# Kernel tuning notes

Measured on AMD Instinct MI355X. Metric: run time of the kernel, lower is better.

The kernel has to match this reference:

```python
import jax, jax.numpy as jnp
import numpy as np

D_MODEL = 1024
NUM_HEADS = 16
D_K = D_MODEL // NUM_HEADS


def setup_inputs() -> dict:
    key = jax.random.key(0)
    ks = jax.random.split(key, 11)
    B, S = 2, 2048
    s = 1.0 / np.sqrt(D_MODEL)
    return {
        "q": jax.random.normal(ks[0], (B, S, D_MODEL), jnp.float32),
        "k": jax.random.normal(ks[1], (B, S, D_MODEL), jnp.float32),
        "v": jax.random.normal(ks[2], (B, S, D_MODEL), jnp.float32),
        "w_q": jax.random.normal(ks[3], (D_MODEL, D_MODEL), jnp.float32) * s,
        "b_q": jnp.zeros((D_MODEL,), jnp.float32),
        "w_k": jax.random.normal(ks[4], (D_MODEL, D_MODEL), jnp.float32) * s,
        "b_k": jnp.zeros((D_MODEL,), jnp.float32),
        "w_v": jax.random.normal(ks[5], (D_MODEL, D_MODEL), jnp.float32) * s,
        "b_v": jnp.zeros((D_MODEL,), jnp.float32),
        "w_o": jax.random.normal(ks[6], (D_MODEL, D_MODEL), jnp.float32) * s,
        "b_o": jnp.zeros((D_MODEL,), jnp.float32),
    }


def reference(q, k, v, w_q, b_q, w_k, b_k, w_v, b_v, w_o, b_o):
    B, S, _ = q.shape
    H, Dk = NUM_HEADS, D_K

    def split_heads(x):  # [B,S,D] -> [B,H,S,Dk]
        return x.reshape(B, S, H, Dk).transpose(0, 2, 1, 3)

    # torch nn.Linear: x @ W.T + b
    qh = split_heads(q @ w_q.T + b_q)
    kh = split_heads(k @ w_k.T + b_k)
    vh = split_heads(v @ w_v.T + b_v)

    scale = 1.0 / jnp.sqrt(jnp.asarray(Dk, qh.dtype))
    scores = jnp.einsum("bhsd,bhtd->bhst", qh, kh) * scale  # [B,H,S,S]
    attn = jax.nn.softmax(scores, axis=-1)
    # dropout is identity in eval/deterministic baseline
    out = jnp.einsum("bhst,bhtd->bhsd", attn, vh)  # [B,H,S,Dk]
    out = out.transpose(0, 2, 1, 3).reshape(B, S, H * Dk)
    return out @ w_o.T + b_o
```

## Files before the change

kernel.cpp:

```cpp
#include <hip/hip_runtime.h>
#include <hip/hip_bf16.h>
#include <stdint.h>

typedef unsigned short u16;
typedef __attribute__((ext_vector_type(8))) short short8;
typedef __attribute__((ext_vector_type(8))) __bf16 bf16x8;
typedef __attribute__((ext_vector_type(4))) float f32x4;
typedef __attribute__((ext_vector_type(4))) uint32_t u32x4;

#if defined(__has_builtin)
#if __has_builtin(__builtin_amdgcn_global_load_lds)
#define USE_GLLDS 1
#endif
#endif

#if defined(__has_builtin)
#if __has_builtin(__builtin_amdgcn_exp2f)
#define HAVE_EXP2_BUILTIN 1
#endif
#endif
__device__ __forceinline__ float fexp2(float x) {
#ifdef HAVE_EXP2_BUILTIN
  return __builtin_amdgcn_exp2f(x);
#else
  return exp2f(x);
#endif
}

__device__ __forceinline__ u16 f2bf(float f) {
  __hip_bfloat16 h = __float2bfloat16(f);
  return __builtin_bit_cast(u16, h);
}

__device__ __forceinline__ f32x4 mfma16(bf16x8 a, bf16x8 b, f32x4 c) {
  return __builtin_amdgcn_mfma_f32_16x16x32_bf16(a, b, c, 0, 0, 0);
}

#ifdef USE_GLLDS
__device__ __forceinline__ void async_cp16(const void* g, void* l) {
  __builtin_amdgcn_global_load_lds(
      (const __attribute__((address_space(1))) void*)g,
      (__attribute__((address_space(3))) void*)l, 16, 0, 0);
}
#endif

__global__ __launch_bounds__(256) void cvt_all(
    const float* __restrict__ q, const float* __restrict__ k,
    const float* __restrict__ v, const float* __restrict__ w0,
    const float* __restrict__ w1, const float* __restrict__ w2,
    const float* __restrict__ w3, u16* __restrict__ dst) {
  size_t i = ((size_t)blockIdx.x * 256 + threadIdx.x) * 8;
  const size_t M1 = 1u << 20;
  const float* s;
  size_t base;
  if (i < 4 * M1) { s = q; base = 0; }
  else if (i < 8 * M1) { s = k; base = 4 * M1; }
  else if (i < 12 * M1) { s = v; base = 8 * M1; }
  else if (i < 13 * M1) { s = w0; base = 12 * M1; }
  else if (i < 14 * M1) { s = w1; base = 13 * M1; }
  else if (i < 15 * M1) { s = w2; base = 14 * M1; }
  else { s = w3; base = 15 * M1; }
  const float4 a = *(const float4*)(s + (i - base));
  const float4 b = *(const float4*)(s + (i - base) + 4);
  short8 r;
  r[0] = (short)f2bf(a.x); r[1] = (short)f2bf(a.y);
  r[2] = (short)f2bf(a.z); r[3] = (short)f2bf(a.w);
  r[4] = (short)f2bf(b.x); r[5] = (short)f2bf(b.y);
  r[6] = (short)f2bf(b.z); r[7] = (short)f2bf(b.w);
  *(short8*)(dst + i) = r;
}

__device__ __forceinline__ void gemm_body(const u16* __restrict__ X,
                                          const u16* __restrict__ W,
                                          const float* __restrict__ bias,
                                          void* __restrict__ outp, int mode) {
  __shared__ u16 Al[128 * 64];
  __shared__ u16 Bl[128 * 64];
  const int tid = threadIdx.x;
  const int wv = tid >> 6, l = tid & 63;
  const int wr = wv >> 1, wc = wv & 1;
  const int m0 = blockIdx.y * 128, n0 = blockIdx.x * 128;
  const int lrow = l & 15, lk = (l >> 4) * 8;

  f32x4 acc[4][4];
#pragma unroll
  for (int i = 0; i < 4; ++i)
#pragma unroll
    for (int j = 0; j < 4; ++j) acc[i][j] = (f32x4){0.f, 0.f, 0.f, 0.f};

  const u16* Asrc = X + (size_t)(m0 + (tid >> 3)) * 1024 + (tid & 7) * 8;
  const u16* Bsrc = W + (size_t)(n0 + (tid >> 3)) * 1024 + (tid & 7) * 8;

  for (int kt = 0; kt < 1024; kt += 64) {
#ifdef USE_GLLDS
#pragma unroll
    for (int p = 0; p < 4; ++p) {
      async_cp16(Asrc + (size_t)p * 32 * 1024 + kt, &Al[p * 2048 + wv * 512]);
      async_cp16(Bsrc + (size_t)p * 32 * 1024 + kt, &Bl[p * 2048 + wv * 512]);
    }
#else
    short8 ar[4], br[4];
#pragma unroll
    for (int p = 0; p < 4; ++p) {
      ar[p] = *(const short8*)(Asrc + (size_t)p * 32 * 1024 + kt);
      br[p] = *(const short8*)(Bsrc + (size_t)p * 32 * 1024 + kt);
    }
#pragma unroll
    for (int p = 0; p < 4; ++p) {
      *(short8*)&Al[p * 2048 + tid * 8] = ar[p];
      *(short8*)&Bl[p * 2048 + tid * 8] = br[p];
    }
#endif
    __syncthreads();
#pragma unroll
    for (int ks = 0; ks < 2; ++ks) {
      bf16x8 af[4], bf[4];
#pragma unroll
      for (int mf = 0; mf < 4; ++mf)
        af[mf] = *(const bf16x8*)&Al[(wr * 64 + mf * 16 + lrow) * 64 + ks * 32 + lk];
#pragma unroll
      for (int nf = 0; nf < 4; ++nf)
        bf[nf] = *(const bf16x8*)&Bl[(wc * 64 + nf * 16 + lrow) * 64 + ks * 32 + lk];
#pragma unroll
      for (int mf = 0; mf < 4; ++mf)
#pragma unroll
        for (int nf = 0; nf < 4; ++nf)
          acc[mf][nf] = mfma16(af[mf], bf[nf], acc[mf][nf]);
    }
    __syncthreads();
  }

  const int rb = (l >> 4) * 4;
#pragma unroll
  for (int mf = 0; mf < 4; ++mf) {
#pragma unroll
    for (int nf = 0; nf < 4; ++nf) {
      const int gn = n0 + wc * 64 + nf * 16 + lrow;
      const float bi = bias[gn];
#pragma unroll
      for (int r = 0; r < 4; ++r) {
        const int gm = m0 + wr * 64 + mf * 16 + rb + r;
        float val = acc[mf][nf][r] + bi;
        const int b = gm >> 11, s = gm & 2047, h = gn >> 6, d = gn & 63;
        if (mode == 3) {
          ((float*)outp)[(size_t)gm * 1024 + gn] = val;
        } else if (mode == 2) {
          ((u16*)outp)[(((size_t)((b * 16 + h) * 64 + d)) << 11) + s] = f2bf(val);
        } else {
          if (mode == 0) val *= 0.18033688f;
          ((u16*)outp)[(((size_t)((b * 16 + h) * 2048 + s)) << 6) + d] = f2bf(val);
        }
      }
    }
  }
}

__global__ __launch_bounds__(256) void gemm_proj(
    const u16* __restrict__ qb, const u16* __restrict__ wqb,
    const float* __restrict__ b_q, const float* __restrict__ b_k,
    const float* __restrict__ b_v, u16* __restrict__ Qh) {
  const int z = blockIdx.z;
  const float* bias = (z == 0) ? b_q : ((z == 1) ? b_k : b_v);
  gemm_body(qb + ((size_t)z << 22), wqb + ((size_t)z << 20), bias,
            Qh + ((size_t)z << 22), z);
}

__global__ __launch_bounds__(256) void gemm_out(
    const u16* __restrict__ X, const u16* __restrict__ W,
    const float* __restrict__ bias, float* __restrict__ out) {
  gemm_body(X, W, bias, out, 3);
}

__global__ __launch_bounds__(512, 4) void flash_attn4(
    const u16* __restrict__ Qh, const u16* __restrict__ Kh,
    const u16* __restrict__ VT, u16* __restrict__ Op,
    float2* __restrict__ ml) {
  __shared__ __align__(16) u16 Kbuf[4096];
  __shared__ __align__(16) u16 Vbuf[4096];
  __shared__ __align__(16) uint32_t Pl[8 * 576];

  const int tid = threadIdx.x;
  const int wv = tid >> 6, l = tid & 63;
  const int q = l & 15, g = l >> 4;

  const int s_lin = blockIdx.x + (blockIdx.y << 4) + (blockIdx.z << 9);
  const int o = ((s_lin & 7) << 7) + (s_lin >> 3);
  const int qt = o & 15, bh = (o >> 4) & 31, z = o >> 9;

  const u16* Qp = Qh + ((size_t)bh * 2048 + qt * 128 + wv * 16) * 64;
  const u16* Kp = Kh + (size_t)bh * 2048 * 64;
  const u16* Vp = VT + (size_t)bh * 64 * 2048;

  bf16x8 qf[2];
  qf[0] = *(const bf16x8*)(Qp + q * 64 + g * 8);
  qf[1] = *(const bf16x8*)(Qp + q * 64 + 32 + g * 8);

  f32x4 o_acc[4];
#pragma unroll
  for (int df = 0; df < 4; ++df) o_acc[df] = (f32x4){0.f, 0.f, 0.f, 0.f};
  float m = -1e30f, ls = 0.f;

  const int srow = l >> 3;
  const int scolq = (l & 7) ^ srow;
  const int pbase = wv * 576 + q * 36;
  const char* kb = (const char*)&Kbuf[0];
  const char* vb = (const char*)&Vbuf[0];
  const int rsw = (q & 7) << 4;

  const u16* kg = Kp + (size_t)(z * 1024 + wv * 8 + srow) * 64 + scolq * 8;
  const u16* vg = Vp + (size_t)(wv * 8 + srow) * 2048 + z * 1024 + scolq * 8;

  {
    short8 k0 = *(const short8*)kg;
    short8 v0 = *(const short8*)vg;
    *(short8*)&Kbuf[wv * 512 + l * 8] = k0;
    *(short8*)&Vbuf[wv * 512 + l * 8] = v0;
  }
  kg += 64 * 64;
  vg += 64;
  __syncthreads();

  for (int tt = 0; tt < 16; ++tt) {
    short8 kr, vr;
    if (tt < 15) {
      kr = *(const short8*)kg;
      vr = *(const short8*)vg;
      kg += 64 * 64;
      vg += 64;
    }

    f32x4 s[4];
#pragma unroll
    for (int nj = 0; nj < 4; ++nj) s[nj] = (f32x4){0.f, 0.f, 0.f, 0.f};
#pragma unroll
    for (int ks = 0; ks < 2; ++ks) {
#pragma unroll
      for (int nj = 0; nj < 4; ++nj) {
        bf16x8 kf = *(const bf16x8*)(kb + (nj * 16 + q) * 128 +
                                     (((ks * 4 + g) << 4) ^ rsw));
        s[nj] = mfma16(kf, qf[ks], s[nj]);
      }
    }

    const float a0 = fmaxf(fmaxf(s[0][0], s[0][1]), fmaxf(s[0][2], s[0][3]));
    const float a1 = fmaxf(fmaxf(s[1][0], s[1][1]), fmaxf(s[1][2], s[1][3]));
    const float a2 = fmaxf(fmaxf(s[2][0], s[2][1]), fmaxf(s[2][2], s[2][3]));
    const float a3 = fmaxf(fmaxf(s[3][0], s[3][1]), fmaxf(s[3][2], s[3][3]));
    float mt = fmaxf(fmaxf(a0, a1), fmaxf(a2, a3));
    mt = fmaxf(mt, __shfl_xor(mt, 16));
    mt = fmaxf(mt, __shfl_xor(mt, 32));
    if (!__all(mt <= m + 8.f)) {
      const float nm = fmaxf(m, mt);
      const float rf = fexp2(m - nm);
      m = nm;
      ls *= rf;
#pragma unroll
      for (int df = 0; df < 4; ++df) o_acc[df] *= rf;
    }
    float ps = 0.f;
#pragma unroll
    for (int nj = 0; nj < 4; ++nj)
#pragma unroll
      for (int r = 0; r < 4; ++r) {
        s[nj][r] = fexp2(s[nj][r] - m);
        ps += s[nj][r];
      }
    ps += __shfl_xor(ps, 16);
    ps += __shfl_xor(ps, 32);
    ls += ps;

#pragma unroll
    for (int nj = 0; nj < 4; ++nj)
#pragma unroll
      for (int pp = 0; pp < 2; ++pp) {
        uint32_t w = (uint32_t)f2bf(s[nj][2 * pp]) |
                     ((uint32_t)f2bf(s[nj][2 * pp + 1]) << 16);
        Pl[pbase + nj * 8 + g * 2 + pp] = w;
      }

#pragma unroll
    for (int ks = 0; ks < 2; ++ks) {
      u32x4 pw = *(const u32x4*)&Pl[pbase + ks * 16 + 4 * g];
      bf16x8 pf = __builtin_bit_cast(bf16x8, pw);
#pragma unroll
      for (int df = 0; df < 4; ++df) {
        bf16x8 vf = *(const bf16x8*)(vb + (df * 16 + q) * 128 +
                                     (((ks * 4 + g) << 4) ^ rsw));
        o_acc[df] = mfma16(vf, pf, o_acc[df]);
      }
    }

    __syncthreads();
    if (tt < 15) {
      *(short8*)&Kbuf[wv * 512 + l * 8] = kr;
      *(short8*)&Vbuf[wv * 512 + l * 8] = vr;
    }
    __syncthreads();
  }

  const float inv = 1.f / ls;
  const int rowb = qt * 128 + wv * 16 + q;
  const size_t prow = (size_t)(z * 32 + bh) * 2048 + rowb;
  u16* Po = Op + (prow << 6);
#pragma unroll
  for (int df = 0; df < 4; ++df)
#pragma unroll
    for (int pp = 0; pp < 2; ++pp) {
      uint32_t w = (uint32_t)f2bf(o_acc[df][2 * pp] * inv) |
                   ((uint32_t)f2bf(o_acc[df][2 * pp + 1] * inv) << 16);
      *(uint32_t*)(Po + df * 16 + 4 * g + 2 * pp) = w;
    }
  if (g == 0) ml[prow] = make_float2(m, ls);
}

__global__ __launch_bounds__(256) void combine(
    const uint32_t* __restrict__ Op32, const float2* __restrict__ ml,
    u16* __restrict__ AO) {
  const int j = blockIdx.x * 256 + threadIdx.x;
  const int rowid = j >> 5, w5 = j & 31;
  const float2 a = ml[rowid];
  const float2 c = ml[(1 << 16) + rowid];
  const float M = fmaxf(a.x, c.x);
  float w1 = a.y * fexp2(a.x - M);
  float w2 = c.y * fexp2(c.x - M);
  const float inv = 1.f / (w1 + w2);
  w1 *= inv;
  w2 *= inv;
  const uint32_t p1 = Op32[j];
  const uint32_t p2 = Op32[(1u << 21) + j];
  const float lo = w1 * __builtin_bit_cast(float, p1 << 16) +
                   w2 * __builtin_bit_cast(float, p2 << 16);
  const float hi = w1 * __builtin_bit_cast(float, p1 & 0xffff0000u) +
                   w2 * __builtin_bit_cast(float, p2 & 0xffff0000u);
  const uint32_t outw = (uint32_t)f2bf(lo) | ((uint32_t)f2bf(hi) << 16);
  const int bh = rowid >> 11, s = rowid & 2047, b = bh >> 4, h = bh & 15;
  ((uint32_t*)AO)[((size_t)(b * 2048 + s) << 9) + h * 32 + w5] = outw;
}

extern "C" void kernel_launch(void* const* d_in, const int* in_sizes, int n_in,
                              void* d_out, int out_size, void* d_ws,
                              size_t ws_size, hipStream_t stream) {
  const float* q = (const float*)d_in[0];
  const float* k = (const float*)d_in[1];
  const float* v = (const float*)d_in[2];
  const float* w_q = (const float*)d_in[3];
  const float* b_q = (const float*)d_in[4];
  const float* w_k = (const float*)d_in[5];
  const float* b_k = (const float*)d_in[6];
  const float* w_v = (const float*)d_in[7];
  const float* b_v = (const float*)d_in[8];
  const float* w_o = (const float*)d_in[9];
  const float* b_o = (const float*)d_in[10];

  u16* ws = (u16*)d_ws;
  u16* qb = ws;
  u16* wqb = ws + (12u << 20);
  u16* wob = ws + (15u << 20);
  u16* Qh = ws + (16u << 20);
  u16* Kh = ws + (20u << 20);
  u16* VT = ws + (24u << 20);
  u16* AO = ws + (28u << 20);
  u16* Op = ws;
  float2* ml = (float2*)(ws + (8u << 20));

  cvt_all<<<dim3(8192), dim3(256), 0, stream>>>(q, k, v, w_q, w_k, w_v, w_o, ws);
  gemm_proj<<<dim3(8, 32, 3), dim3(256), 0, stream>>>(qb, wqb, b_q, b_k, b_v, Qh);
  flash_attn4<<<dim3(16, 32, 2), dim3(512), 0, stream>>>(Qh, Kh, VT, Op, ml);
  combine<<<dim3(8192), dim3(256), 0, stream>>>((const uint32_t*)Op, ml, AO);
  gemm_out<<<dim3(8, 32), dim3(256), 0, stream>>>(AO, wob, b_o, (float*)d_out);
}
```

Measured before the change: 172.2 us.

## Double-buffer GEMM LDS tiles and remap blocks for XCD L2 locality

The projection and output GEMMs now use two LDS buffers, so the next k-tile's global-to-LDS copy is issued before the MFMA work on the current tile. This replaces one of the two barriers per iteration and is meant to hide load latency. The grids are flattened to 1D, and block IDs are remapped so each XCD works on a contiguous patch of M×N tiles, aiming to improve L2 reuse of weights and activations. Launch bounds now request 2 blocks per CU, while doubling LDS to 64 KB per block limits occupancy.

```diff
diff --git a/kernel.cpp b/kernel.cpp
--- a/kernel.cpp
+++ b/kernel.cpp
@@ -70,16 +70,16 @@
   *(short8*)(dst + i) = r;
 }
 
-__device__ __forceinline__ void gemm_body(const u16* __restrict__ X,
+__device__ __forceinline__ void gemm_core(const u16* __restrict__ X,
                                           const u16* __restrict__ W,
                                           const float* __restrict__ bias,
-                                          void* __restrict__ outp, int mode) {
-  __shared__ u16 Al[128 * 64];
-  __shared__ u16 Bl[128 * 64];
+                                          void* __restrict__ outp, int mode,
+                                          int m0, int n0) {
+  __shared__ u16 Al[2][128 * 64];
+  __shared__ u16 Bl[2][128 * 64];
   const int tid = threadIdx.x;
   const int wv = tid >> 6, l = tid & 63;
   const int wr = wv >> 1, wc = wv & 1;
-  const int m0 = blockIdx.y * 128, n0 = blockIdx.x * 128;
   const int lrow = l & 15, lk = (l >> 4) * 8;
 
   f32x4 acc[4][4];
@@ -89,38 +89,53 @@
     for (int j = 0; j < 4; ++j) acc[i][j] = (f32x4){0.f, 0.f, 0.f, 0.f};
 
   const u16* Asrc = X + (size_t)(m0 + (tid >> 3)) * 1024 + (tid & 7) * 8;
-  const u16* Bsrc = W + (size_t)(n0 + (tid >> 3)) * 1024 + (tid & 7) * 8;
+  const u16* Bsrc = W + (size_t)(tid >> 3) * 1024 + (tid & 7) * 8;
+
+#ifdef USE_GLLDS
+#define GSTAGE(buf, kt)                                                       \
+  do {                                                                        \
+    _Pragma("unroll")                                                         \
+    for (int p = 0; p < 4; ++p) {                                             \
+      async_cp16(Asrc + (size_t)p * 32 * 1024 + (kt),                         \
+                 &Al[buf][p * 2048 + wv * 512]);                              \
+      async_cp16(Bsrc + (size_t)p * 32 * 1024 + (kt),                         \
+                 &Bl[buf][p * 2048 + wv * 512]);                              \
+    }                                                                         \
+  } while (0)
+#else
+#define GSTAGE(buf, kt)                                                       \
+  do {                                                                        \
+    short8 ar_[4], br_[4];                                                    \
+    _Pragma("unroll")                                                         \
+    for (int p = 0; p < 4; ++p) {                                             \
+      ar_[p] = *(const short8*)(Asrc + (size_t)p * 32 * 1024 + (kt));         \
+      br_[p] = *(const short8*)(Bsrc + (size_t)p * 32 * 1024 + (kt));         \
+    }                                                                         \
+    _Pragma("unroll")                                                         \
+    for (int p = 0; p < 4; ++p) {                                             \
+      *(short8*)&Al[buf][p * 2048 + tid * 8] = ar_[p];                        \
+      *(short8*)&Bl[buf][p * 2048 + tid * 8] = br_[p];                        \
+    }                                                                         \
+  } while (0)
+#endif
+
+  GSTAGE(0, 0);
+  __syncthreads();
 
   for (int kt = 0; kt < 1024; kt += 64) {
-#ifdef USE_GLLDS
-#pragma unroll
-    for (int p = 0; p < 4; ++p) {
-      async_cp16(Asrc + (size_t)p * 32 * 1024 + kt, &Al[p * 2048 + wv * 512]);
-      async_cp16(Bsrc + (size_t)p * 32 * 1024 + kt, &Bl[p * 2048 + wv * 512]);
-    }
-#else
-    short8 ar[4], br[4];
-#pragma unroll
-    for (int p = 0; p < 4; ++p) {
-      ar[p] = *(const short8*)(Asrc + (size_t)p * 32 * 1024 + kt);
-      br[p] = *(const short8*)(Bsrc + (size_t)p * 32 * 1024 + kt);
-    }
-#pragma unroll
-    for (int p = 0; p < 4; ++p) {
-      *(short8*)&Al[p * 2048 + tid * 8] = ar[p];
-      *(short8*)&Bl[p * 2048 + tid * 8] = br[p];
-    }
-#endif
-    __syncthreads();
+    const int cur = (kt >> 6) & 1;
+    if (kt < 1024 - 64) GSTAGE(cur ^ 1, kt + 64);
 #pragma unroll
     for (int ks = 0; ks < 2; ++ks) {
       bf16x8 af[4], bf[4];
 #pragma unroll
       for (int mf = 0; mf < 4; ++mf)
-        af[mf] = *(const bf16x8*)&Al[(wr * 64 + mf * 16 + lrow) * 64 + ks * 32 + lk];
+        af[mf] = *(const bf16x8*)&Al[cur][(wr * 64 + mf * 16 + lrow) * 64 +
+                                         ks * 32 + lk];
 #pragma unroll
       for (int nf = 0; nf < 4; ++nf)
-        bf[nf] = *(const bf16x8*)&Bl[(wc * 64 + nf * 16 + lrow) * 64 + ks * 32 + lk];
+        bf[nf] = *(const bf16x8*)&Bl[cur][(wc * 64 + nf * 16 + lrow) * 64 +
+                                          ks * 32 + lk];
 #pragma unroll
       for (int mf = 0; mf < 4; ++mf)
 #pragma unroll
@@ -129,6 +144,7 @@
     }
     __syncthreads();
   }
+#undef GSTAGE
 
   const int rb = (l >> 4) * 4;
 #pragma unroll
@@ -155,20 +171,28 @@
   }
 }
 
-__global__ __launch_bounds__(256) void gemm_proj(
+__global__ __launch_bounds__(256, 2) void gemm_proj(
     const u16* __restrict__ qb, const u16* __restrict__ wqb,
     const float* __restrict__ b_q, const float* __restrict__ b_k,
     const float* __restrict__ b_v, u16* __restrict__ Qh) {
-  const int z = blockIdx.z;
+  const int s = blockIdx.x;
+  const int xcd = s & 7, c = s >> 3;
+  const int nx = (xcd >> 2) * 12 + (c % 12);
+  const int my = (xcd & 3) * 8 + (c / 12);
+  const int z = nx >> 3, nxl = nx & 7;
   const float* bias = (z == 0) ? b_q : ((z == 1) ? b_k : b_v);
-  gemm_body(qb + ((size_t)z << 22), wqb + ((size_t)z << 20), bias,
-            Qh + ((size_t)z << 22), z);
-}
-
-__global__ __launch_bounds__(256) void gemm_out(
+  gemm_core(qb + ((size_t)z << 22), wqb + ((size_t)nx << 17), bias,
+            Qh + ((size_t)z << 22), z, my * 128, nxl * 128);
+}
+
+__global__ __launch_bounds__(256, 2) void gemm_out(
     const u16* __restrict__ X, const u16* __restrict__ W,
     const float* __restrict__ bias, float* __restrict__ out) {
-  gemm_body(X, W, bias, out, 3);
+  const int s = blockIdx.x;
+  const int xcd = s & 7, c = s >> 3;
+  const int nx = (xcd >> 2) * 4 + (c & 3);
+  const int my = (xcd & 3) * 8 + (c >> 2);
+  gemm_core(X, W + ((size_t)nx << 17), bias, out, 3, my * 128, nx * 128);
 }
 
 __global__ __launch_bounds__(512, 4) void flash_attn4(
@@ -364,8 +388,8 @@
   float2* ml = (float2*)(ws + (8u << 20));
 
   cvt_all<<<dim3(8192), dim3(256), 0, stream>>>(q, k, v, w_q, w_k, w_v, w_o, ws);
-  gemm_proj<<<dim3(8, 32, 3), dim3(256), 0, stream>>>(qb, wqb, b_q, b_k, b_v, Qh);
+  gemm_proj<<<dim3(768), dim3(256), 0, stream>>>(qb, wqb, b_q, b_k, b_v, Qh);
   flash_attn4<<<dim3(16, 32, 2), dim3(512), 0, stream>>>(Qh, Kh, VT, Op, ml);
   combine<<<dim3(8192), dim3(256), 0, stream>>>((const uint32_t*)Op, ml, AO);
-  gemm_out<<<dim3(8, 32), dim3(256), 0, stream>>>(AO, wob, b_o, (float*)d_out);
-}
+  gemm_out<<<dim3(256), dim3(256), 0, stream>>>(AO, wob, b_o, (float*)d_out);
+}
```

New measurement: 164.8 us. 4.3% less time.
